# Kernel tuning notes

Measured on AMD Instinct MI355X. Metric: run time of the kernel, lower is better.

Reference implementation:

```python
import jax, jax.numpy as jnp
import numpy as np

N = 100000
E = 1600000
D = 128
L = 3  # num_layers
EPS = 1e-5


def setup_inputs() -> dict:
    key = jax.random.key(0)
    ks = jax.random.split(key, 10)
    feat = jax.random.normal(ks[0], (N, D), dtype=jnp.float32)
    src = jax.random.randint(ks[1], (E,), 0, N, dtype=jnp.int32)
    dst = jax.random.randint(ks[2], (E,), 0, N, dtype=jnp.int32)
    s = 1.0 / np.sqrt(D)
    W_pool = jax.random.uniform(ks[3], (L, D, D), jnp.float32, -s, s)
    b_pool = jax.random.uniform(ks[4], (L, D), jnp.float32, -s, s)
    W_self = jax.random.uniform(ks[5], (L, D, D), jnp.float32, -s, s)
    W_neigh = jax.random.uniform(ks[6], (L, D, D), jnp.float32, -s, s)
    bias = jnp.zeros((L, D), jnp.float32)
    gamma = jnp.ones((L, D), jnp.float32)
    beta = jnp.zeros((L, D), jnp.float32)
    return {"feat": feat, "W_pool": W_pool, "b_pool": b_pool, "W_self": W_self,
            "W_neigh": W_neigh, "bias": bias, "gamma": gamma, "beta": beta,
            "src": src, "dst": dst}


def _sage_pool_layer(h, Wp, bp, Ws, Wn, b, src_all, dst_all):
    # DGL SAGEConv(aggregator_type='pool'):
    # h_pool = relu(fc_pool(h)); neigh = max over in-edges of h_pool[src];
    # out = fc_self(h) + fc_neigh(neigh) + bias  (fc_self/fc_neigh bias-free)
    hp = jax.nn.relu(h @ Wp + bp)                      # [N, d]
    msgs = hp[src_all]                                  # [E+N, d] gather
    neigh = jax.ops.segment_max(msgs, dst_all, num_segments=N)  # [N, d]
    return h @ Ws + neigh @ Wn + b


def _bn_relu(x, g, b):
    # BatchNorm1d in training mode (batch stats, biased variance) + ReLU
    mean = jnp.mean(x, axis=0)
    var = jnp.mean(jnp.square(x - mean), axis=0)
    return jax.nn.relu((x - mean) * jax.lax.rsqrt(var + EPS) * g + b)


def reference(feat, W_pool, b_pool, W_self, W_neigh, bias, gamma, beta, src, dst):
    # dgl.add_self_loop
    loop = jnp.arange(N, dtype=src.dtype)
    src_all = jnp.concatenate([src, loop])
    dst_all = jnp.concatenate([dst, loop])
    h = feat
    for l in range(L):
        h = _sage_pool_layer(h, W_pool[l], b_pool[l], W_self[l], W_neigh[l],
                             bias[l], src_all, dst_all)
        h = _bn_relu(h, gamma[l], beta[l])
    return h
```

## Files before the change

kernel.cpp:

```cpp
#include <hip/hip_runtime.h>

#define DD 128
#define MAXB 256
#define BSH 9
#define PEB 4096
#define RB 64
#define CAP 10240

typedef unsigned short u16;
typedef unsigned int   u32;
typedef __attribute__((ext_vector_type(8))) short bf16x8;
typedef __attribute__((ext_vector_type(4))) float f32x4;

union U8 { uint4 u; bf16x8 v; };

__device__ inline u16 f2bf(float x) {
  u32 u = __float_as_uint(x);
  u += 0x7fffu + ((u >> 16) & 1u);
  return (u16)(u >> 16);
}
__device__ inline float bf2f_lo(u32 w) { return __uint_as_float(w << 16); }
__device__ inline float bf2f_hi(u32 w) { return __uint_as_float(w & 0xffff0000u); }

__device__ inline u32 pkmax(u32 a, u32 b) {
  u32 r;
  asm("v_pk_max_u16 %0, %1, %2" : "=v"(r) : "v"(a), "v"(b));
  return r;
}

__device__ inline uint4 fragF32(const float* __restrict__ p) {
  float4 a = *(const float4*)p;
  float4 b = *(const float4*)(p + 4);
  uint4 o;
  o.x = (u32)f2bf(a.x) | ((u32)f2bf(a.y) << 16);
  o.y = (u32)f2bf(a.z) | ((u32)f2bf(a.w) << 16);
  o.z = (u32)f2bf(b.x) | ((u32)f2bf(b.y) << 16);
  o.w = (u32)f2bf(b.z) | ((u32)f2bf(b.w) << 16);
  return o;
}

__device__ inline uint4 fragBN(const u16* __restrict__ p,
                               const float* __restrict__ sc,
                               const float* __restrict__ sh, int k0) {
  uint4 u = *(const uint4*)p;
  float4 c0 = *(const float4*)(sc + k0);
  float4 c1 = *(const float4*)(sc + k0 + 4);
  float4 h0 = *(const float4*)(sh + k0);
  float4 h1 = *(const float4*)(sh + k0 + 4);
  float y0 = fmaxf(fmaf(bf2f_lo(u.x), c0.x, h0.x), 0.f);
  float y1 = fmaxf(fmaf(bf2f_hi(u.x), c0.y, h0.y), 0.f);
  float y2 = fmaxf(fmaf(bf2f_lo(u.y), c0.z, h0.z), 0.f);
  float y3 = fmaxf(fmaf(bf2f_hi(u.y), c0.w, h0.w), 0.f);
  float y4 = fmaxf(fmaf(bf2f_lo(u.z), c1.x, h1.x), 0.f);
  float y5 = fmaxf(fmaf(bf2f_hi(u.z), c1.y, h1.y), 0.f);
  float y6 = fmaxf(fmaf(bf2f_lo(u.w), c1.z, h1.z), 0.f);
  float y7 = fmaxf(fmaf(bf2f_hi(u.w), c1.w, h1.w), 0.f);
  uint4 o;
  o.x = (u32)f2bf(y0) | ((u32)f2bf(y1) << 16);
  o.y = (u32)f2bf(y2) | ((u32)f2bf(y3) << 16);
  o.z = (u32)f2bf(y4) | ((u32)f2bf(y5) << 16);
  o.w = (u32)f2bf(y6) | ((u32)f2bf(y7) << 16);
  return o;
}

__global__ __launch_bounds__(256) void k_pack_w(
    const float* __restrict__ Wp, const float* __restrict__ Wsf,
    const float* __restrict__ Wn, u16* __restrict__ Wpk)
{
  int g = blockIdx.x * 256 + threadIdx.x;
  int m = g >> 11;
  if (m >= 9) return;
  int t = g & 2047;
  const float* W = (m < 3) ? Wp + (size_t)m * 16384
                 : (m < 6) ? Wsf + (size_t)(m - 3) * 16384
                           : Wn + (size_t)(m - 6) * 16384;
  int ks = t >> 9, nt = (t >> 6) & 7, l = t & 63;
  int kbase = ks * 32 + (l >> 4) * 8;
  int n = nt * 16 + (l & 15);
  u32 o[4];
#pragma unroll
  for (int p = 0; p < 4; p++) {
    u16 e0 = f2bf(W[(size_t)(kbase + 2 * p) * DD + n]);
    u16 e1 = f2bf(W[(size_t)(kbase + 2 * p + 1) * DD + n]);
    o[p] = (u32)e0 | ((u32)e1 << 16);
  }
  uint4* dst = (uint4*)(Wpk + (size_t)m * 16384 + (size_t)t * 8);
  *dst = make_uint4(o[0], o[1], o[2], o[3]);
}

template<int MODE>
__global__ __launch_bounds__(256, 4) void k_gemm_pool(
    const float* __restrict__ featf, const u16* __restrict__ xb,
    const u16* __restrict__ Wpk, const float* __restrict__ bvec,
    const float* __restrict__ sc, const float* __restrict__ sh,
    u16* __restrict__ hp, int nrows)
{
  const int tid = threadIdx.x;
  const int w = tid >> 6, l = tid & 63;
  const int lg = l >> 4, lm = l & 15;
  const int m0 = blockIdx.x * 128 + w * 32;

  f32x4 acc[2][8];
#pragma unroll
  for (int a = 0; a < 2; a++)
#pragma unroll
    for (int b = 0; b < 8; b++) acc[a][b] = (f32x4){0.f, 0.f, 0.f, 0.f};

  int n0 = m0 + lm;      if (n0 >= nrows) n0 = nrows - 1;
  int n1 = m0 + 16 + lm; if (n1 >= nrows) n1 = nrows - 1;
  const u16* wl = Wpk + l * 8;

#pragma unroll
  for (int ks = 0; ks < 4; ks++) {
    const int k0 = ks * 32 + lg * 8;
    U8 a0, a1;
    if (MODE == 0) {
      a0.u = fragF32(featf + (size_t)n0 * DD + k0);
      a1.u = fragF32(featf + (size_t)n1 * DD + k0);
    } else {
      a0.u = fragBN(xb + (size_t)n0 * DD + k0, sc, sh, k0);
      a1.u = fragBN(xb + (size_t)n1 * DD + k0, sc, sh, k0);
    }
#pragma unroll
    for (int nt = 0; nt < 8; nt++) {
      bf16x8 wf = *(const bf16x8*)(wl + (ks * 8 + nt) * 512);
      acc[0][nt] = __builtin_amdgcn_mfma_f32_16x16x32_bf16(wf, a0.v, acc[0][nt], 0, 0, 0);
      acc[1][nt] = __builtin_amdgcn_mfma_f32_16x16x32_bf16(wf, a1.v, acc[1][nt], 0, 0, 0);
    }
  }

#pragma unroll
  for (int mf = 0; mf < 2; mf++) {
    int node = m0 + mf * 16 + lm;
    if (node < nrows) {
      u16* dst = hp + (size_t)node * DD + lg * 4;
#pragma unroll
      for (int nt = 0; nt < 8; nt++) {
        float4 b4 = *(const float4*)(bvec + nt * 16 + lg * 4);
        f32x4 a = acc[mf][nt];
        float v0 = fmaxf(a[0] + b4.x, 0.f);
        float v1 = fmaxf(a[1] + b4.y, 0.f);
        float v2 = fmaxf(a[2] + b4.z, 0.f);
        float v3 = fmaxf(a[3] + b4.w, 0.f);
        uint2 o;
        o.x = (u32)f2bf(v0) | ((u32)f2bf(v1) << 16);
        o.y = (u32)f2bf(v2) | ((u32)f2bf(v3) << 16);
        *(uint2*)(dst + nt * 16) = o;
      }
    }
  }
}

template<int MODE>
__global__ __launch_bounds__(256, 4) void k_gemm_out(
    const float* __restrict__ featf, u16* xb,
    const u16* __restrict__ gb,
    const u16* __restrict__ WpkS, const u16* __restrict__ WpkN,
    const float* __restrict__ bvec,
    const float* __restrict__ sc, const float* __restrict__ sh,
    float* __restrict__ parts, int nrows)
{
  __shared__ float red[64 * 132];
  const int tid = threadIdx.x;
  const int w = tid >> 6, l = tid & 63;
  const int lg = l >> 4, lm = l & 15;
  const int m0 = blockIdx.x * 128 + w * 32;

  f32x4 acc[2][8];
#pragma unroll
  for (int a = 0; a < 2; a++)
#pragma unroll
    for (int b = 0; b < 8; b++) acc[a][b] = (f32x4){0.f, 0.f, 0.f, 0.f};

  int n0 = m0 + lm;      if (n0 >= nrows) n0 = nrows - 1;
  int n1 = m0 + 16 + lm; if (n1 >= nrows) n1 = nrows - 1;

#pragma unroll
  for (int ks = 0; ks < 4; ks++) {
    const int k0 = ks * 32 + lg * 8;
    U8 a0, a1;
    if (MODE == 0) {
      a0.u = fragF32(featf + (size_t)n0 * DD + k0);
      a1.u = fragF32(featf + (size_t)n1 * DD + k0);
    } else {
      a0.u = fragBN(xb + (size_t)n0 * DD + k0, sc, sh, k0);
      a1.u = fragBN(xb + (size_t)n1 * DD + k0, sc, sh, k0);
    }
    const u16* wl = WpkS + l * 8;
#pragma unroll
    for (int nt = 0; nt < 8; nt++) {
      bf16x8 wf = *(const bf16x8*)(wl + (ks * 8 + nt) * 512);
      acc[0][nt] = __builtin_amdgcn_mfma_f32_16x16x32_bf16(wf, a0.v, acc[0][nt], 0, 0, 0);
      acc[1][nt] = __builtin_amdgcn_mfma_f32_16x16x32_bf16(wf, a1.v, acc[1][nt], 0, 0, 0);
    }
  }
#pragma unroll
  for (int ks = 0; ks < 4; ks++) {
    const int k0 = ks * 32 + lg * 8;
    bf16x8 g0 = *(const bf16x8*)(gb + (size_t)n0 * DD + k0);
    bf16x8 g1 = *(const bf16x8*)(gb + (size_t)n1 * DD + k0);
    const u16* wl = WpkN + l * 8;
#pragma unroll
    for (int nt = 0; nt < 8; nt++) {
      bf16x8 wf = *(const bf16x8*)(wl + (ks * 8 + nt) * 512);
      acc[0][nt] = __builtin_amdgcn_mfma_f32_16x16x32_bf16(wf, g0, acc[0][nt], 0, 0, 0);
      acc[1][nt] = __builtin_amdgcn_mfma_f32_16x16x32_bf16(wf, g1, acc[1][nt], 0, 0, 0);
    }
  }

  const float msk0 = (m0 + lm < nrows) ? 1.f : 0.f;
  const float msk1 = (m0 + 16 + lm < nrows) ? 1.f : 0.f;
#pragma unroll
  for (int nt = 0; nt < 8; nt++) {
    float4 b4 = *(const float4*)(bvec + nt * 16 + lg * 4);
    acc[0][nt][0] += b4.x; acc[0][nt][1] += b4.y;
    acc[0][nt][2] += b4.z; acc[0][nt][3] += b4.w;
    acc[1][nt][0] += b4.x; acc[1][nt][1] += b4.y;
    acc[1][nt][2] += b4.z; acc[1][nt][3] += b4.w;
  }
#pragma unroll
  for (int mf = 0; mf < 2; mf++) {
    int node = m0 + mf * 16 + lm;
    if (node < nrows) {
      u16* dst = xb + (size_t)node * DD + lg * 4;
#pragma unroll
      for (int nt = 0; nt < 8; nt++) {
        f32x4 a = acc[mf][nt];
        uint2 o;
        o.x = (u32)f2bf(a[0]) | ((u32)f2bf(a[1]) << 16);
        o.y = (u32)f2bf(a[2]) | ((u32)f2bf(a[3]) << 16);
        *(uint2*)(dst + nt * 16) = o;
      }
    }
  }

  const int rowbase = (w * 16 + lm) * 132;
#pragma unroll
  for (int nt = 0; nt < 8; nt++) {
    float4 sv;
    sv.x = msk0 * acc[0][nt][0] + msk1 * acc[1][nt][0];
    sv.y = msk0 * acc[0][nt][1] + msk1 * acc[1][nt][1];
    sv.z = msk0 * acc[0][nt][2] + msk1 * acc[1][nt][2];
    sv.w = msk0 * acc[0][nt][3] + msk1 * acc[1][nt][3];
    *(float4*)&red[rowbase + nt * 16 + lg * 4] = sv;
  }
  __syncthreads();
  float ssum = 0.f;
  if (tid < 128) {
#pragma unroll
    for (int r = 0; r < 64; r++) ssum += red[r * 132 + tid];
  }
  __syncthreads();
#pragma unroll
  for (int nt = 0; nt < 8; nt++) {
    float4 qv;
    qv.x = msk0 * acc[0][nt][0] * acc[0][nt][0] + msk1 * acc[1][nt][0] * acc[1][nt][0];
    qv.y = msk0 * acc[0][nt][1] * acc[0][nt][1] + msk1 * acc[1][nt][1] * acc[1][nt][1];
    qv.z = msk0 * acc[0][nt][2] * acc[0][nt][2] + msk1 * acc[1][nt][2] * acc[1][nt][2];
    qv.w = msk0 * acc[0][nt][3] * acc[0][nt][3] + msk1 * acc[1][nt][3] * acc[1][nt][3];
    *(float4*)&red[rowbase + nt * 16 + lg * 4] = qv;
  }
  __syncthreads();
  if (tid < 128) {
    float qsum = 0.f;
#pragma unroll
    for (int r = 0; r < 64; r++) qsum += red[r * 132 + tid];
    parts[(size_t)blockIdx.x * 256 + tid] = ssum;
    parts[(size_t)blockIdx.x * 256 + 128 + tid] = qsum;
  }
}

__global__ __launch_bounds__(256) void k_red1(
    const float* __restrict__ parts, float* __restrict__ pp, int nblk)
{
  int t = threadIdx.x;
  float s = 0.f;
  for (int r = blockIdx.x; r < nblk; r += RB) s += parts[(size_t)r * 256 + t];
  pp[blockIdx.x * 256 + t] = s;
}

__global__ void k_init(int* __restrict__ bcur, int* __restrict__ bcnt) {
  int i = threadIdx.x;
  bcur[i] = i * CAP;
  bcnt[i] = 0;
}

__global__ __launch_bounds__(256) void k_part(
    const int* __restrict__ src, const int* __restrict__ dst,
    int* __restrict__ bcur, int* __restrict__ bcnt,
    u32* __restrict__ pairs, int E)
{
  __shared__ int cnt[MAXB];
  __shared__ int base[MAXB];
  const int e0 = blockIdx.x * PEB;
  int s[16], d[16];
#pragma unroll
  for (int k = 0; k < 16; k++) {
    int e = e0 + threadIdx.x + k * 256;
    bool ok = (e < E);
    s[k] = ok ? src[e] : 0;
    d[k] = ok ? dst[e] : -1;
  }
  for (int i = threadIdx.x; i < MAXB; i += 256) cnt[i] = 0;
  __syncthreads();
#pragma unroll
  for (int k = 0; k < 16; k++)
    if (d[k] >= 0) atomicAdd(&cnt[d[k] >> BSH], 1);
  __syncthreads();
  for (int i = threadIdx.x; i < MAXB; i += 256) {
    int c = cnt[i];
    if (c) { base[i] = atomicAdd(&bcur[i], c); atomicAdd(&bcnt[i], c); }
    cnt[i] = 0;
  }
  __syncthreads();
#pragma unroll
  for (int k = 0; k < 16; k++) {
    if (d[k] >= 0) {
      int b = d[k] >> BSH;
      int r = atomicAdd(&cnt[b], 1);
      pairs[base[b] + r] = ((u32)s[k] << 9) | (u32)(d[k] & 511);
    }
  }
}

__global__ __launch_bounds__(256) void k_csr(
    const u32* __restrict__ pairs, const int* __restrict__ bcnt,
    int2* __restrict__ offend, int* __restrict__ eidx, int nrows)
{
  __shared__ int cnt[512];
  __shared__ int ps[256];
  const int b = blockIdx.x;
  const int lo = b * CAP;
  const int hi = lo + bcnt[b];
  const int t = threadIdx.x;
  cnt[t] = 0; cnt[t + 256] = 0;
  __syncthreads();
  for (int i = lo + t; i < hi; i += 256)
    atomicAdd(&cnt[pairs[i] & 511], 1);
  __syncthreads();
  int c0 = cnt[2 * t], c1 = cnt[2 * t + 1];
  ps[t] = c0 + c1;
  __syncthreads();
  int acc = ps[t];
#pragma unroll
  for (int s = 1; s < 256; s <<= 1) {
    int u = (t >= s) ? ps[t - s] : 0;
    __syncthreads();
    acc += u;
    ps[t] = acc;
    __syncthreads();
  }
  int base = lo + acc - (c0 + c1);
  int node0 = (b << BSH) + 2 * t;
  if (node0 < nrows)     offend[node0]     = make_int2(base, base + c0);
  if (node0 + 1 < nrows) offend[node0 + 1] = make_int2(base + c0, base + c0 + c1);
  cnt[2 * t]     = base;
  cnt[2 * t + 1] = base + c0;
  __syncthreads();
  for (int i = lo + t; i < hi; i += 256) {
    u32 p = pairs[i];
    int pos = atomicAdd(&cnt[p & 511], 1);
    eidx[pos] = (int)(p >> 9);
  }
}

__global__ __launch_bounds__(256, 8) void k_aggregate(
    const uint4* __restrict__ hp4, const int2* __restrict__ offend,
    const int* __restrict__ eidx, uint4* __restrict__ nb4, int nrows)
{
  int d = blockIdx.x * 4 + (threadIdx.x >> 6);
  if (d >= nrows) return;
  const int l = threadIdx.x & 63;
  const int part = l & 15;
  const int slot = l >> 4;
  uint4 a = hp4[(size_t)d * 16 + part];
  const int2 oe = offend[d];
  const int b = oe.x, e = oe.y;
  const int len = (e - b + 3) >> 2;
  int i = b + slot * len;
  const int i1 = min(i + len, e);
  for (; i + 3 < i1; i += 4) {
    int s0 = eidx[i], s1 = eidx[i + 1], s2 = eidx[i + 2], s3 = eidx[i + 3];
    uint4 v0 = hp4[(size_t)s0 * 16 + part];
    uint4 v1 = hp4[(size_t)s1 * 16 + part];
    uint4 v2 = hp4[(size_t)s2 * 16 + part];
    uint4 v3 = hp4[(size_t)s3 * 16 + part];
    a.x = pkmax(pkmax(a.x, pkmax(v0.x, v1.x)), pkmax(v2.x, v3.x));
    a.y = pkmax(pkmax(a.y, pkmax(v0.y, v1.y)), pkmax(v2.y, v3.y));
    a.z = pkmax(pkmax(a.z, pkmax(v0.z, v1.z)), pkmax(v2.z, v3.z));
    a.w = pkmax(pkmax(a.w, pkmax(v0.w, v1.w)), pkmax(v2.w, v3.w));
  }
  if (i < i1) {
    int s0 = eidx[i];
    int s1 = (i + 1 < i1) ? eidx[i + 1] : s0;
    int s2 = (i + 2 < i1) ? eidx[i + 2] : s0;
    uint4 v0 = hp4[(size_t)s0 * 16 + part];
    uint4 v1 = hp4[(size_t)s1 * 16 + part];
    uint4 v2 = hp4[(size_t)s2 * 16 + part];
    a.x = pkmax(pkmax(a.x, v0.x), pkmax(v1.x, v2.x));
    a.y = pkmax(pkmax(a.y, v0.y), pkmax(v1.y, v2.y));
    a.z = pkmax(pkmax(a.z, v0.z), pkmax(v1.z, v2.z));
    a.w = pkmax(pkmax(a.w, v0.w), pkmax(v1.w, v2.w));
  }
  a.x = pkmax(a.x, (u32)__shfl_xor((int)a.x, 16, 64));
  a.y = pkmax(a.y, (u32)__shfl_xor((int)a.y, 16, 64));
  a.z = pkmax(a.z, (u32)__shfl_xor((int)a.z, 16, 64));
  a.w = pkmax(a.w, (u32)__shfl_xor((int)a.w, 16, 64));
  a.x = pkmax(a.x, (u32)__shfl_xor((int)a.x, 32, 64));
  a.y = pkmax(a.y, (u32)__shfl_xor((int)a.y, 32, 64));
  a.z = pkmax(a.z, (u32)__shfl_xor((int)a.z, 32, 64));
  a.w = pkmax(a.w, (u32)__shfl_xor((int)a.w, 32, 64));
  if (slot == 0) nb4[(size_t)d * 16 + part] = a;
}

__global__ __launch_bounds__(256) void k_bn_prep(
    const float* __restrict__ pp,
    const float* __restrict__ gamma, const float* __restrict__ beta,
    float* __restrict__ sc, float* __restrict__ sh, float invN)
{
  __shared__ float sums[256];
  int t = threadIdx.x;
  float s = 0.f;
#pragma unroll
  for (int k = 0; k < RB; k++) s += pp[k * 256 + t];
  sums[t] = s;
  __syncthreads();
  if (t < 128) {
    float mean = sums[t] * invN;
    float var  = sums[128 + t] * invN - mean * mean;
    float g = gamma[t] * rsqrtf(var + 1e-5f);
    sc[t] = g;
    sh[t] = beta[t] - mean * g;
  }
}

__global__ __launch_bounds__(256) void k_bn_final(
    const u16* __restrict__ xb, float* __restrict__ out,
    const float* __restrict__ sc, const float* __restrict__ sh, int n8)
{
  int i = blockIdx.x * 256 + threadIdx.x;
  if (i >= n8) return;
  uint4 v = ((const uint4*)xb)[i];
  int f0 = (i & 15) * 8;
  float4 c0 = *(const float4*)(sc + f0);
  float4 c1 = *(const float4*)(sc + f0 + 4);
  float4 h0 = *(const float4*)(sh + f0);
  float4 h1 = *(const float4*)(sh + f0 + 4);
  float4* o = (float4*)out + 2 * (size_t)i;
  o[0] = make_float4(fmaxf(fmaf(bf2f_lo(v.x), c0.x, h0.x), 0.f),
                     fmaxf(fmaf(bf2f_hi(v.x), c0.y, h0.y), 0.f),
                     fmaxf(fmaf(bf2f_lo(v.y), c0.z, h0.z), 0.f),
                     fmaxf(fmaf(bf2f_hi(v.y), c0.w, h0.w), 0.f));
  o[1] = make_float4(fmaxf(fmaf(bf2f_lo(v.z), c1.x, h1.x), 0.f),
                     fmaxf(fmaf(bf2f_hi(v.z), c1.y, h1.y), 0.f),
                     fmaxf(fmaf(bf2f_lo(v.w), c1.z, h1.z), 0.f),
                     fmaxf(fmaf(bf2f_hi(v.w), c1.w, h1.w), 0.f));
}

extern "C" void kernel_launch(void* const* d_in, const int* in_sizes, int n_in,
                              void* d_out, int out_size, void* d_ws, size_t ws_size,
                              hipStream_t stream)
{
  const float* feat    = (const float*)d_in[0];
  const float* W_pool  = (const float*)d_in[1];
  const float* b_pool  = (const float*)d_in[2];
  const float* W_self  = (const float*)d_in[3];
  const float* W_neigh = (const float*)d_in[4];
  const float* bias    = (const float*)d_in[5];
  const float* gamma   = (const float*)d_in[6];
  const float* beta    = (const float*)d_in[7];
  const int*   src     = (const int*)d_in[8];
  const int*   dst     = (const int*)d_in[9];

  const int Nn = in_sizes[0] / DD;
  const int E  = in_sizes[8];
  float* out = (float*)d_out;

  const int gB = (Nn + 127) / 128;

  const size_t ND = (size_t)Nn * DD;
  u16*   xb    = (u16*)d_ws;
  u16*   hp    = xb + ND;
  u16*   nbuf  = hp + ND;
  u16*   Wpk   = nbuf + ND;
  float* sc    = (float*)(Wpk + 9 * 16384);
  float* sh    = sc + 128;
  float* pp    = sh + 128;
  float* parts = pp + RB * 256;
  int*   bcnt  = (int*)(parts + (size_t)gB * 256);
  int*   bcur  = bcnt + MAXB;
  int2*  offend = (int2*)(bcur + MAXB);
  const int nbuk = (Nn + 511) >> BSH;
  u32*   pairs = (u32*)(offend + Nn);
  int*   eidx  = (int*)(pairs + (size_t)nbuk * CAP);

  const int pB   = (E + PEB - 1) / PEB;
  const int aggB = (Nn + 3) / 4;
  const int n8   = Nn * (DD / 8);
  const int cB   = (n8 + 255) / 256;

  k_pack_w<<<72, 256, 0, stream>>>(W_pool, W_self, W_neigh, Wpk);
  k_init<<<1, MAXB, 0, stream>>>(bcur, bcnt);
  k_part<<<pB, 256, 0, stream>>>(src, dst, bcur, bcnt, pairs, E);
  k_csr<<<nbuk, 256, 0, stream>>>(pairs, bcnt, offend, eidx, Nn);

  for (int l = 0; l < 3; l++) {
    const float* bp = b_pool + (size_t)l * DD;
    const float* bl = bias + (size_t)l * DD;
    const u16* WP = Wpk + (size_t)l * 16384;
    const u16* WS = Wpk + (size_t)(3 + l) * 16384;
    const u16* WN = Wpk + (size_t)(6 + l) * 16384;

    if (l == 0)
      k_gemm_pool<0><<<gB, 256, 0, stream>>>(feat, nullptr, WP, bp, sc, sh, hp, Nn);
    else
      k_gemm_pool<1><<<gB, 256, 0, stream>>>(nullptr, xb, WP, bp, sc, sh, hp, Nn);

    k_aggregate<<<aggB, 256, 0, stream>>>((const uint4*)hp, offend, eidx, (uint4*)nbuf, Nn);

    if (l == 0)
      k_gemm_out<0><<<gB, 256, 0, stream>>>(feat, xb, nbuf, WS, WN, bl, sc, sh, parts, Nn);
    else
      k_gemm_out<1><<<gB, 256, 0, stream>>>(nullptr, xb, nbuf, WS, WN, bl, sc, sh, parts, Nn);

    k_red1<<<RB, 256, 0, stream>>>(parts, pp, gB);
    k_bn_prep<<<1, 256, 0, stream>>>(pp, gamma + (size_t)l * DD,
                                     beta + (size_t)l * DD, sc, sh, 1.0f / (float)Nn);
  }
  k_bn_final<<<cB, 256, 0, stream>>>(xb, out, sc, sh, n8);
  (void)n_in; (void)out_size; (void)ws_size;
}
```

Before: 432.9 us.

## Move BatchNorm statistics out of GEMM epilogue into separate streaming stats kernel

The sum and sum-of-squares reduction, which used a 33KB LDS buffer and several barriers, is removed from the output GEMM epilogue. A new k_stats kernel instead re-reads the bf16 layer output to compute per-feature partials, and k_red1 is dropped. The buffer-init kernel is folded into the weight-packing launch as an extra block. This frees LDS in the GEMM, which may raise occupancy, at the cost of an extra 25MB read per layer, and the statistics are now computed from bf16-rounded values rather than fp32 accumulators.

```diff
diff --git a/kernel.cpp b/kernel.cpp
--- a/kernel.cpp
+++ b/kernel.cpp
@@ -4,7 +4,7 @@
 #define MAXB 256
 #define BSH 9
 #define PEB 4096
-#define RB 64
+#define SB 128
 #define CAP 10240
 
 typedef unsigned short u16;
@@ -65,8 +65,15 @@
 
 __global__ __launch_bounds__(256) void k_pack_w(
     const float* __restrict__ Wp, const float* __restrict__ Wsf,
-    const float* __restrict__ Wn, u16* __restrict__ Wpk)
-{
+    const float* __restrict__ Wn, u16* __restrict__ Wpk,
+    int* __restrict__ bcur, int* __restrict__ bcnt)
+{
+  if (blockIdx.x == 72) {
+    int i = threadIdx.x;
+    bcur[i] = i * CAP;
+    bcnt[i] = 0;
+    return;
+  }
   int g = blockIdx.x * 256 + threadIdx.x;
   int m = g >> 11;
   if (m >= 9) return;
@@ -158,9 +165,8 @@
     const u16* __restrict__ WpkS, const u16* __restrict__ WpkN,
     const float* __restrict__ bvec,
     const float* __restrict__ sc, const float* __restrict__ sh,
-    float* __restrict__ parts, int nrows)
-{
-  __shared__ float red[64 * 132];
+    int nrows)
+{
   const int tid = threadIdx.x;
   const int w = tid >> 6, l = tid & 63;
   const int lg = l >> 4, lm = l & 15;
@@ -208,16 +214,6 @@
     }
   }
 
-  const float msk0 = (m0 + lm < nrows) ? 1.f : 0.f;
-  const float msk1 = (m0 + 16 + lm < nrows) ? 1.f : 0.f;
-#pragma unroll
-  for (int nt = 0; nt < 8; nt++) {
-    float4 b4 = *(const float4*)(bvec + nt * 16 + lg * 4);
-    acc[0][nt][0] += b4.x; acc[0][nt][1] += b4.y;
-    acc[0][nt][2] += b4.z; acc[0][nt][3] += b4.w;
-    acc[1][nt][0] += b4.x; acc[1][nt][1] += b4.y;
-    acc[1][nt][2] += b4.z; acc[1][nt][3] += b4.w;
-  }
 #pragma unroll
   for (int mf = 0; mf < 2; mf++) {
     int node = m0 + mf * 16 + lm;
@@ -225,64 +221,79 @@
       u16* dst = xb + (size_t)node * DD + lg * 4;
 #pragma unroll
       for (int nt = 0; nt < 8; nt++) {
+        float4 b4 = *(const float4*)(bvec + nt * 16 + lg * 4);
         f32x4 a = acc[mf][nt];
         uint2 o;
-        o.x = (u32)f2bf(a[0]) | ((u32)f2bf(a[1]) << 16);
-        o.y = (u32)f2bf(a[2]) | ((u32)f2bf(a[3]) << 16);
+        o.x = (u32)f2bf(a[0] + b4.x) | ((u32)f2bf(a[1] + b4.y) << 16);
+        o.y = (u32)f2bf(a[2] + b4.z) | ((u32)f2bf(a[3] + b4.w) << 16);
         *(uint2*)(dst + nt * 16) = o;
       }
     }
   }
-
-  const int rowbase = (w * 16 + lm) * 132;
-#pragma unroll
-  for (int nt = 0; nt < 8; nt++) {
-    float4 sv;
-    sv.x = msk0 * acc[0][nt][0] + msk1 * acc[1][nt][0];
-    sv.y = msk0 * acc[0][nt][1] + msk1 * acc[1][nt][1];
-    sv.z = msk0 * acc[0][nt][2] + msk1 * acc[1][nt][2];
-    sv.w = msk0 * acc[0][nt][3] + msk1 * acc[1][nt][3];
-    *(float4*)&red[rowbase + nt * 16 + lg * 4] = sv;
-  }
-  __syncthreads();
-  float ssum = 0.f;
-  if (tid < 128) {
-#pragma unroll
-    for (int r = 0; r < 64; r++) ssum += red[r * 132 + tid];
-  }
-  __syncthreads();
-#pragma unroll
-  for (int nt = 0; nt < 8; nt++) {
-    float4 qv;
-    qv.x = msk0 * acc[0][nt][0] * acc[0][nt][0] + msk1 * acc[1][nt][0] * acc[1][nt][0];
-    qv.y = msk0 * acc[0][nt][1] * acc[0][nt][1] + msk1 * acc[1][nt][1] * acc[1][nt][1];
-    qv.z = msk0 * acc[0][nt][2] * acc[0][nt][2] + msk1 * acc[1][nt][2] * acc[1][nt][2];
-    qv.w = msk0 * acc[0][nt][3] * acc[0][nt][3] + msk1 * acc[1][nt][3] * acc[1][nt][3];
-    *(float4*)&red[rowbase + nt * 16 + lg * 4] = qv;
-  }
-  __syncthreads();
-  if (tid < 128) {
-    float qsum = 0.f;
-#pragma unroll
-    for (int r = 0; r < 64; r++) qsum += red[r * 132 + tid];
-    parts[(size_t)blockIdx.x * 256 + tid] = ssum;
-    parts[(size_t)blockIdx.x * 256 + 128 + tid] = qsum;
-  }
-}
-
-__global__ __launch_bounds__(256) void k_red1(
-    const float* __restrict__ parts, float* __restrict__ pp, int nblk)
-{
+}
+
+__global__ __launch_bounds__(256) void k_stats(
+    const u16* __restrict__ xb, float* __restrict__ parts, int nchunks)
+{
+  __shared__ float sm[256][8];
+  int t = threadIdx.x;
+  float s[8], q[8];
+#pragma unroll
+  for (int j = 0; j < 8; j++) { s[j] = 0.f; q[j] = 0.f; }
+  for (int i = blockIdx.x * 256 + t; i < nchunks; i += gridDim.x * 256) {
+    uint4 v = ((const uint4*)xb)[i];
+    float f;
+    f = bf2f_lo(v.x); s[0] += f; q[0] += f * f;
+    f = bf2f_hi(v.x); s[1] += f; q[1] += f * f;
+    f = bf2f_lo(v.y); s[2] += f; q[2] += f * f;
+    f = bf2f_hi(v.y); s[3] += f; q[3] += f * f;
+    f = bf2f_lo(v.z); s[4] += f; q[4] += f * f;
+    f = bf2f_hi(v.z); s[5] += f; q[5] += f * f;
+    f = bf2f_lo(v.w); s[6] += f; q[6] += f * f;
+    f = bf2f_hi(v.w); s[7] += f; q[7] += f * f;
+  }
+#pragma unroll
+  for (int j = 0; j < 8; j++) sm[t][j] = s[j];
+  __syncthreads();
+  if (t < 128) {
+    int fc = t >> 3, j = t & 7;
+    float a = 0.f;
+#pragma unroll
+    for (int g = 0; g < 16; g++) a += sm[g * 16 + fc][j];
+    parts[blockIdx.x * 256 + t] = a;
+  }
+  __syncthreads();
+#pragma unroll
+  for (int j = 0; j < 8; j++) sm[t][j] = q[j];
+  __syncthreads();
+  if (t < 128) {
+    int fc = t >> 3, j = t & 7;
+    float a = 0.f;
+#pragma unroll
+    for (int g = 0; g < 16; g++) a += sm[g * 16 + fc][j];
+    parts[blockIdx.x * 256 + 128 + t] = a;
+  }
+}
+
+__global__ __launch_bounds__(256) void k_bn_prep(
+    const float* __restrict__ parts,
+    const float* __restrict__ gamma, const float* __restrict__ beta,
+    float* __restrict__ sc, float* __restrict__ sh, float invN)
+{
+  __shared__ float sums[256];
   int t = threadIdx.x;
   float s = 0.f;
-  for (int r = blockIdx.x; r < nblk; r += RB) s += parts[(size_t)r * 256 + t];
-  pp[blockIdx.x * 256 + t] = s;
-}
-
-__global__ void k_init(int* __restrict__ bcur, int* __restrict__ bcnt) {
-  int i = threadIdx.x;
-  bcur[i] = i * CAP;
-  bcnt[i] = 0;
+#pragma unroll 8
+  for (int k = 0; k < SB; k++) s += parts[k * 256 + t];
+  sums[t] = s;
+  __syncthreads();
+  if (t < 128) {
+    float mean = sums[t] * invN;
+    float var  = sums[128 + t] * invN - mean * mean;
+    float g = gamma[t] * rsqrtf(var + 1e-5f);
+    sc[t] = g;
+    sh[t] = beta[t] - mean * g;
+  }
 }
 
 __global__ __launch_bounds__(256) void k_part(
@@ -413,27 +424,6 @@
   if (slot == 0) nb4[(size_t)d * 16 + part] = a;
 }
 
-__global__ __launch_bounds__(256) void k_bn_prep(
-    const float* __restrict__ pp,
-    const float* __restrict__ gamma, const float* __restrict__ beta,
-    float* __restrict__ sc, float* __restrict__ sh, float invN)
-{
-  __shared__ float sums[256];
-  int t = threadIdx.x;
-  float s = 0.f;
-#pragma unroll
-  for (int k = 0; k < RB; k++) s += pp[k * 256 + t];
-  sums[t] = s;
-  __syncthreads();
-  if (t < 128) {
-    float mean = sums[t] * invN;
-    float var  = sums[128 + t] * invN - mean * mean;
-    float g = gamma[t] * rsqrtf(var + 1e-5f);
-    sc[t] = g;
-    sh[t] = beta[t] - mean * g;
-  }
-}
-
 __global__ __launch_bounds__(256) void k_bn_final(
     const u16* __restrict__ xb, float* __restrict__ out,
     const float* __restrict__ sc, const float* __restrict__ sh, int n8)
@@ -485,9 +475,8 @@
   u16*   Wpk   = nbuf + ND;
   float* sc    = (float*)(Wpk + 9 * 16384);
   float* sh    = sc + 128;
-  float* pp    = sh + 128;
-  float* parts = pp + RB * 256;
-  int*   bcnt  = (int*)(parts + (size_t)gB * 256);
+  float* parts = sh + 128;
+  int*   bcnt  = (int*)(parts + SB * 256);
   int*   bcur  = bcnt + MAXB;
   int2*  offend = (int2*)(bcur + MAXB);
   const int nbuk = (Nn + 511) >> BSH;
@@ -499,8 +488,7 @@
   const int n8   = Nn * (DD / 8);
   const int cB   = (n8 + 255) / 256;
 
-  k_pack_w<<<72, 256, 0, stream>>>(W_pool, W_self, W_neigh, Wpk);
-  k_init<<<1, MAXB, 0, stream>>>(bcur, bcnt);
+  k_pack_w<<<73, 256, 0, stream>>>(W_pool, W_self, W_neigh, Wpk, bcur, bcnt);
   k_part<<<pB, 256, 0, stream>>>(src, dst, bcur, bcnt, pairs, E);
   k_csr<<<nbuk, 256, 0, stream>>>(pairs, bcnt, offend, eidx, Nn);
 
@@ -519,12 +507,12 @@
     k_aggregate<<<aggB, 256, 0, stream>>>((const uint4*)hp, offend, eidx, (uint4*)nbuf, Nn);
 
     if (l == 0)
-      k_gemm_out<0><<<gB, 256, 0, stream>>>(feat, xb, nbuf, WS, WN, bl, sc, sh, parts, Nn);
+      k_gemm_out<0><<<gB, 256, 0, stream>>>(feat, xb, nbuf, WS, WN, bl, sc, sh, Nn);
     else
-      k_gemm_out<1><<<gB, 256, 0, stream>>>(nullptr, xb, nbuf, WS, WN, bl, sc, sh, parts, Nn);
-
-    k_red1<<<RB, 256, 0, stream>>>(parts, pp, gB);
-    k_bn_prep<<<1, 256, 0, stream>>>(pp, gamma + (size_t)l * DD,
+      k_gemm_out<1><<<gB, 256, 0, stream>>>(nullptr, xb, nbuf, WS, WN, bl, sc, sh, Nn);
+
+    k_stats<<<SB, 256, 0, stream>>>(xb, parts, Nn * 16);
+    k_bn_prep<<<1, 256, 0, stream>>>(parts, gamma + (size_t)l * DD,
                                      beta + (size_t)l * DD, sc, sh, 1.0f / (float)Nn);
   }
   k_bn_final<<<cB, 256, 0, stream>>>(xb, out, sc, sh, n8);
```

Measured after the change: 470.6 us. 8.7% more time.
